# Performance work log

Hardware: AMD Instinct MI355X
Metric: run time of the kernel (lower is better)

The kernel has to match this reference:

```python
import jax, jax.numpy as jnp
import numpy as np

B, N, E = 32, 256, 300   # batch, num hyperedges, word emb size
H, K = 256, 8            # nhidden, nhead
MARGIN = 0.2


def setup_inputs() -> dict:
    key = jax.random.key(0)
    ks = jax.random.split(key, 10)
    s_in = 1.0 / np.sqrt(E)
    s_h = 1.0 / np.sqrt(H)
    s_fc = 1.0 / np.sqrt(H * K)
    return {
        'he_anchor': jax.random.normal(ks[0], (B, N, E), jnp.float32),
        'he_pos': jax.random.normal(ks[1], (B, N, E), jnp.float32),
        'he_neg': jax.random.normal(ks[2], (B, N, E), jnp.float32),
        'W_a2h': jax.random.uniform(ks[3], (H, E), jnp.float32, -s_in, s_in),
        'b_a2h': jax.random.uniform(ks[4], (H,), jnp.float32, -s_in, s_in),
        'W_c2h': jax.random.uniform(ks[5], (H, E), jnp.float32, -s_in, s_in),
        'b_c2h': jax.random.uniform(ks[6], (H,), jnp.float32, -s_in, s_in),
        'W_att': jax.random.uniform(ks[7], (K, H), jnp.float32, -s_h, s_h),
        'b_att': jax.random.uniform(ks[8], (K,), jnp.float32, -s_h, s_h),
        'W_fc': jax.random.uniform(ks[9], (1, H * K), jnp.float32, -s_fc, s_fc),
        'b_fc': jnp.zeros((1,), jnp.float32),
    }


def _score(x, y, W_a2h, b_a2h, W_c2h, b_c2h, W_att, b_att, W_fc, b_fc):
    # a2h / c2h projections, then permute to [B, H, N]
    Aa = jnp.transpose(x @ W_a2h.T + b_a2h, (0, 2, 1))  # [B,H,N]
    Ac = jnp.transpose(y @ W_c2h.T + b_c2h, (0, 2, 1))  # [B,H,M]
    # h2att applied to the outer product Aa[b,h,n]*Ac[b,h,m]; fuse into one einsum
    logits = jnp.einsum('bhn,bhm,kh->bknm', Aa, Ac, W_att) + b_att[None, :, None, None]
    b_, k_, n_, m_ = logits.shape
    att = jax.nn.softmax(logits.reshape(b_, k_, n_ * m_), axis=-1).reshape(b_, k_, n_, m_)
    # per-head bilinear aggregation: out[b,k,h] = sum_{n,m} Aa[b,h,n]*att[b,k,n,m]*Ac[b,h,m]
    t = jnp.einsum('bhn,bknm->bkhm', Aa, att)
    out = jnp.einsum('bkhm,bhm->bkh', t, Ac)
    # torch concat order is head-major: [B, K*H]
    out = out.reshape(b_, k_ * H)
    return out @ W_fc.T + b_fc  # [B,1]


def reference(he_anchor, he_pos, he_neg, W_a2h, b_a2h, W_c2h, b_c2h, W_att, b_att, W_fc, b_fc):
    score_p = _score(he_anchor, he_pos, W_a2h, b_a2h, W_c2h, b_c2h, W_att, b_att, W_fc, b_fc)
    score_n = _score(he_anchor, he_neg, W_a2h, b_a2h, W_c2h, b_c2h, W_att, b_att, W_fc, b_fc)
    loss = jnp.mean(jax.nn.relu(score_n - score_p + MARGIN))
    return loss
```

## Files before the change

kernel.cpp:

```cpp
#include <hip/hip_runtime.h>

#define BB 32
#define NN 256
#define EE 300
#define HH 256
#define KK 8
#define MARGINF 0.2f

typedef __attribute__((ext_vector_type(8))) short bf16x8;
typedef __attribute__((ext_vector_type(4))) float f32x4;
typedef __attribute__((ext_vector_type(16))) float f32x16;

__device__ inline ushort f2bf(float f) {
  unsigned u = __float_as_uint(f);
  u += 0x7fffu + ((u >> 16) & 1u);
  return (ushort)(u >> 16);
}
__device__ inline float bf2f(ushort s) { return __uint_as_float(((unsigned)s) << 16); }
__device__ inline unsigned pack2bf(float f0, float f1) {
  unsigned u0 = __float_as_uint(f0); u0 += 0x7fffu + ((u0 >> 16) & 1u);
  unsigned u1 = __float_as_uint(f1); u1 += 0x7fffu + ((u1 >> 16) & 1u);
  return (u0 >> 16) | (u1 & 0xffff0000u);
}

__global__ __launch_bounds__(256, 3) void proj_kernel(
    const float* __restrict__ he_a, const float* __restrict__ he_p,
    const float* __restrict__ he_n,
    const float* __restrict__ W_a2h, const float* __restrict__ b_a2h,
    const float* __restrict__ W_c2h, const float* __restrict__ b_c2h,
    ushort* __restrict__ AT)
{
  const int z = blockIdx.y;
  const int which = z >> 5;
  const int b = z & 31;
  const int n0 = blockIdx.x * 32;
  const int tid = threadIdx.x;
  const int wv = tid >> 6;
  const int lane = tid & 63;
  const int col = lane & 15;
  const int quad = lane >> 4;

  const float* X = (which == 0 ? he_a : which == 1 ? he_p : he_n) + (size_t)b * NN * EE;
  const float* W = (which == 0 ? W_a2h : W_c2h);
  const float* bias = (which == 0 ? b_a2h : b_c2h);

  __shared__ __align__(16) ushort sX[32][72];
  __shared__ __align__(16) ushort sW[256][72];
  ushort (*tr)[264] = (ushort (*)[264])&sW[0][0];

  f32x4 acc[2][4];
#pragma unroll
  for (int nf = 0; nf < 2; nf++)
#pragma unroll
    for (int mb = 0; mb < 4; mb++) acc[nf][mb] = (f32x4){0.f, 0.f, 0.f, 0.f};

  const int c4 = tid & 15;
  const int rbase = tid >> 4;

  for (int c = 0; c < 5; c++) {
    __syncthreads();
    const int e = 64 * c + 4 * c4;
    const bool ok = (e < 300);
    {
#pragma unroll
      for (int q = 0; q < 2; q++) {
        const int row = rbase + 16 * q;
        float4 xv = {0.f, 0.f, 0.f, 0.f};
        if (ok) xv = *(const float4*)&X[(size_t)(n0 + row) * EE + e];
        uint2 p; p.x = pack2bf(xv.x, xv.y); p.y = pack2bf(xv.z, xv.w);
        *(uint2*)&sX[row][c4 * 4] = p;
      }
    }
    {
#pragma unroll
      for (int q = 0; q < 16; q++) {
        const int row = rbase + 16 * q;
        float4 wf = {0.f, 0.f, 0.f, 0.f};
        if (ok) wf = *(const float4*)&W[(size_t)row * EE + e];
        uint2 p; p.x = pack2bf(wf.x, wf.y); p.y = pack2bf(wf.z, wf.w);
        *(uint2*)&sW[row][c4 * 4] = p;
      }
    }
    __syncthreads();
#pragma unroll
    for (int ks = 0; ks < 2; ks++) {
      const int off = 32 * ks + 8 * quad;
      const bf16x8 a0 = *(const bf16x8*)&sX[col][off];
      const bf16x8 a1 = *(const bf16x8*)&sX[16 + col][off];
#pragma unroll
      for (int mb = 0; mb < 4; mb++) {
        const bf16x8 wb = *(const bf16x8*)&sW[64 * wv + 16 * mb + col][off];
        acc[0][mb] = __builtin_amdgcn_mfma_f32_16x16x32_bf16(a0, wb, acc[0][mb], 0, 0, 0);
        acc[1][mb] = __builtin_amdgcn_mfma_f32_16x16x32_bf16(a1, wb, acc[1][mb], 0, 0, 0);
      }
    }
  }

  __syncthreads();
#pragma unroll
  for (int nf = 0; nf < 2; nf++)
#pragma unroll
    for (int mb = 0; mb < 4; mb++) {
      const float bi = bias[64 * wv + 16 * mb + col];
#pragma unroll
      for (int r = 0; r < 4; r++)
        tr[16 * nf + 4 * quad + r][64 * wv + 16 * mb + col] = f2bf(acc[nf][mb][r] + bi);
    }
  __syncthreads();
  {
    const int row = tid >> 3, seg = tid & 7;
    ushort* dst = &AT[((size_t)(which * BB + b) * NN + n0 + row) * HH];
#pragma unroll
    for (int j = 0; j < 4; j++)
      *(uint4*)&dst[(seg * 4 + j) * 8] = *(const uint4*)&tr[row][(seg * 4 + j) * 8];
  }
}

__global__ __launch_bounds__(256, 2) void attn_kernel(
    const ushort* __restrict__ AT, const float* __restrict__ Watt,
    const float* __restrict__ Wfc, float* __restrict__ scoresK)
{
  const int idx = blockIdx.x;
  const int k = idx >> 6;
  const int g = idx & 63;
  const int which = g >> 5;
  const int b = g & 31;
  const int tid = threadIdx.x;
  const int wv = tid >> 6;
  const int lane = tid & 63;
  const int row32 = lane & 31;
  const int half32 = lane >> 5;

  const ushort* At_a = AT + (size_t)b * NN * HH;
  const ushort* At_c = AT + ((size_t)(1 + which) * BB + b) * NN * HH;
  const uint4* Ac_u4 = (const uint4*)At_c;

  __shared__ __align__(16) ushort sAc[64][264];
  __shared__ __align__(16) float wkf[256];
  __shared__ __align__(16) float wff[256];
  __shared__ float red[8];

  wkf[tid] = Watt[(size_t)k * HH + tid];
  wff[tid] = Wfc[(size_t)k * HH + tid];
  __syncthreads();

  float num = 0.f, den = 0.f;
  const int srow = tid >> 5, scol8 = (tid & 31) * 8;

  for (int s = 0; s < 2; s++) {
    const int nbase = 128 * s + 32 * wv;
    bf16x8 saf[16], gaf[16];
    const ushort* arow = At_a + (size_t)(nbase + row32) * HH;
#pragma unroll
    for (int ks = 0; ks < 16; ks++) {
      const int off = 16 * ks + 8 * half32;
      const bf16x8 a = *(const bf16x8*)&arow[off];
      const float4 wa = *(const float4*)&wkf[off];
      const float4 wb = *(const float4*)&wkf[off + 4];
      const float4 fa = *(const float4*)&wff[off];
      const float4 fb = *(const float4*)&wff[off + 4];
      const float w[8] = {wa.x, wa.y, wa.z, wa.w, wb.x, wb.y, wb.z, wb.w};
      const float f[8] = {fa.x, fa.y, fa.z, fa.w, fb.x, fb.y, fb.z, fb.w};
      union { bf16x8 v; unsigned u[4]; } sv, gv;
#pragma unroll
      for (int jj = 0; jj < 4; jj++) {
        const float a0 = bf2f((ushort)a[2 * jj]), a1 = bf2f((ushort)a[2 * jj + 1]);
        sv.u[jj] = pack2bf(a0 * w[2 * jj], a1 * w[2 * jj + 1]);
        gv.u[jj] = pack2bf(a0 * f[2 * jj], a1 * f[2 * jj + 1]);
      }
      saf[ks] = sv.v; gaf[ks] = gv.v;
    }

    for (int mc = 0; mc < 4; mc++) {
      __syncthreads();
#pragma unroll
      for (int q = 0; q < 8; q++) {
        const int row = q * 8 + srow;
        *(uint4*)&sAc[row][scol8] = Ac_u4[(size_t)(64 * mc + row) * 32 + (tid & 31)];
      }
      __syncthreads();

      f32x16 aS0 = {0,0,0,0,0,0,0,0,0,0,0,0,0,0,0,0};
      f32x16 aS1 = {0,0,0,0,0,0,0,0,0,0,0,0,0,0,0,0};
      f32x16 aG0 = {0,0,0,0,0,0,0,0,0,0,0,0,0,0,0,0};
      f32x16 aG1 = {0,0,0,0,0,0,0,0,0,0,0,0,0,0,0,0};
#pragma unroll
      for (int ks = 0; ks < 16; ks++) {
        const int off = 16 * ks + 8 * half32;
        const bf16x8 b0 = *(const bf16x8*)&sAc[row32][off];
        const bf16x8 b1 = *(const bf16x8*)&sAc[32 + row32][off];
        aS0 = __builtin_amdgcn_mfma_f32_32x32x16_bf16(saf[ks], b0, aS0, 0, 0, 0);
        aG0 = __builtin_amdgcn_mfma_f32_32x32x16_bf16(gaf[ks], b0, aG0, 0, 0, 0);
        aS1 = __builtin_amdgcn_mfma_f32_32x32x16_bf16(saf[ks], b1, aS1, 0, 0, 0);
        aG1 = __builtin_amdgcn_mfma_f32_32x32x16_bf16(gaf[ks], b1, aG1, 0, 0, 0);
      }
#pragma unroll
      for (int r = 0; r < 16; r++) {
        const float p0 = __expf(aS0[r]);
        den += p0; num += p0 * aG0[r];
        const float p1 = __expf(aS1[r]);
        den += p1; num += p1 * aG1[r];
      }
    }
  }

#pragma unroll
  for (int off = 32; off >= 1; off >>= 1) {
    num += __shfl_xor(num, off);
    den += __shfl_xor(den, off);
  }
  if (lane == 0) { red[wv] = num; red[4 + wv] = den; }
  __syncthreads();
  if (tid == 0) {
    const float nt = red[0] + red[1] + red[2] + red[3];
    const float dt = red[4] + red[5] + red[6] + red[7];
    scoresK[idx] = nt / dt;
  }
}

__global__ __launch_bounds__(64) void loss_kernel(
    const float* __restrict__ scoresK, const float* __restrict__ bfc,
    float* __restrict__ out)
{
  const int tid = threadIdx.x;
  float s = bfc[0];
#pragma unroll
  for (int k = 0; k < KK; k++) s += scoresK[k * 64 + tid];
  const float other = __shfl(s, tid + 32);
  float v = 0.f;
  if (tid < 32) v = fmaxf(other - s + MARGINF, 0.f);
#pragma unroll
  for (int off = 32; off >= 1; off >>= 1) v += __shfl_xor(v, off);
  if (tid == 0) out[0] = v * (1.0f / 32.0f);
}

extern "C" void kernel_launch(void* const* d_in, const int* in_sizes, int n_in,
                              void* d_out, int out_size, void* d_ws, size_t ws_size,
                              hipStream_t stream) {
  const float* he_a  = (const float*)d_in[0];
  const float* he_p  = (const float*)d_in[1];
  const float* he_n  = (const float*)d_in[2];
  const float* W_a2h = (const float*)d_in[3];
  const float* b_a2h = (const float*)d_in[4];
  const float* W_c2h = (const float*)d_in[5];
  const float* b_c2h = (const float*)d_in[6];
  const float* W_att = (const float*)d_in[7];
  const float* W_fc  = (const float*)d_in[9];
  const float* b_fc  = (const float*)d_in[10];

  ushort* AT = (ushort*)d_ws;
  float* scoresK = (float*)(AT + (size_t)3 * BB * NN * HH);
  (void)ws_size; (void)in_sizes; (void)n_in; (void)out_size;

  dim3 pg(8, 96);
  proj_kernel<<<pg, 256, 0, stream>>>(he_a, he_p, he_n, W_a2h, b_a2h, W_c2h, b_c2h, AT);
  attn_kernel<<<512, 256, 0, stream>>>(AT, W_att, W_fc, scoresK);
  loss_kernel<<<1, 64, 0, stream>>>(scoresK, b_fc, (float*)d_out);
}
```

Before: 162.8 us.

## Pre-convert projection weights to padded bf16 and read them directly from global

Adds a small kernel that converts W_a2h and W_c2h once per call into a bf16 buffer padded to 320 columns. The projection kernel now loads the whole 32x300 X tile into shared memory up front, then streams weight fragments straight from global/L2 into the MFMAs, with no per-chunk weight staging or barriers. This removes the fp32 weight loads and their conversion, which every one of the 768 blocks used to repeat. The costs are an extra kernel launch, and weight fragments now come from global/L2 with no shared-memory reuse.

```diff
diff --git a/kernel.cpp b/kernel.cpp
--- a/kernel.cpp
+++ b/kernel.cpp
@@ -6,6 +6,7 @@
 #define HH 256
 #define KK 8
 #define MARGINF 0.2f
+#define EP 320
 
 typedef __attribute__((ext_vector_type(8))) short bf16x8;
 typedef __attribute__((ext_vector_type(4))) float f32x4;
@@ -23,11 +24,23 @@
   return (u0 >> 16) | (u1 & 0xffff0000u);
 }
 
+__global__ __launch_bounds__(256) void wconv_kernel(
+    const float* __restrict__ Wa, const float* __restrict__ Wc,
+    ushort* __restrict__ Wb)
+{
+  const int i = blockIdx.x * 256 + threadIdx.x;
+  const int e = i % EP;
+  const int hw = i / EP;
+  const int h = hw & 255;
+  const int w = hw >> 8;
+  const float* src = w ? Wc : Wa;
+  Wb[i] = (e < EE) ? f2bf(src[(size_t)h * EE + e]) : (ushort)0;
+}
+
 __global__ __launch_bounds__(256, 3) void proj_kernel(
     const float* __restrict__ he_a, const float* __restrict__ he_p,
-    const float* __restrict__ he_n,
-    const float* __restrict__ W_a2h, const float* __restrict__ b_a2h,
-    const float* __restrict__ W_c2h, const float* __restrict__ b_c2h,
+    const float* __restrict__ he_n, const ushort* __restrict__ Wb,
+    const float* __restrict__ b_a2h, const float* __restrict__ b_c2h,
     ushort* __restrict__ AT)
 {
   const int z = blockIdx.y;
@@ -41,12 +54,25 @@
   const int quad = lane >> 4;
 
   const float* X = (which == 0 ? he_a : which == 1 ? he_p : he_n) + (size_t)b * NN * EE;
-  const float* W = (which == 0 ? W_a2h : W_c2h);
+  const ushort* W = Wb + (size_t)(which == 0 ? 0 : 1) * HH * EP;
   const float* bias = (which == 0 ? b_a2h : b_c2h);
 
-  __shared__ __align__(16) ushort sX[32][72];
-  __shared__ __align__(16) ushort sW[256][72];
-  ushort (*tr)[264] = (ushort (*)[264])&sW[0][0];
+  __shared__ __align__(16) ushort sX[32][328];
+  __shared__ __align__(16) ushort tr[32][264];
+
+  {
+    const int row = tid >> 3, seg = tid & 7;
+    const float* xr = X + (size_t)(n0 + row) * EE;
+#pragma unroll
+    for (int q = 0; q < 10; q++) {
+      const int j = seg + 8 * q;
+      float4 xv = {0.f, 0.f, 0.f, 0.f};
+      if (j < 75) xv = *(const float4*)&xr[4 * j];
+      uint2 p; p.x = pack2bf(xv.x, xv.y); p.y = pack2bf(xv.z, xv.w);
+      *(uint2*)&sX[row][4 * j] = p;
+    }
+  }
+  __syncthreads();
 
   f32x4 acc[2][4];
 #pragma unroll
@@ -54,49 +80,19 @@
 #pragma unroll
     for (int mb = 0; mb < 4; mb++) acc[nf][mb] = (f32x4){0.f, 0.f, 0.f, 0.f};
 
-  const int c4 = tid & 15;
-  const int rbase = tid >> 4;
-
-  for (int c = 0; c < 5; c++) {
-    __syncthreads();
-    const int e = 64 * c + 4 * c4;
-    const bool ok = (e < 300);
-    {
-#pragma unroll
-      for (int q = 0; q < 2; q++) {
-        const int row = rbase + 16 * q;
-        float4 xv = {0.f, 0.f, 0.f, 0.f};
-        if (ok) xv = *(const float4*)&X[(size_t)(n0 + row) * EE + e];
-        uint2 p; p.x = pack2bf(xv.x, xv.y); p.y = pack2bf(xv.z, xv.w);
-        *(uint2*)&sX[row][c4 * 4] = p;
-      }
-    }
-    {
-#pragma unroll
-      for (int q = 0; q < 16; q++) {
-        const int row = rbase + 16 * q;
-        float4 wf = {0.f, 0.f, 0.f, 0.f};
-        if (ok) wf = *(const float4*)&W[(size_t)row * EE + e];
-        uint2 p; p.x = pack2bf(wf.x, wf.y); p.y = pack2bf(wf.z, wf.w);
-        *(uint2*)&sW[row][c4 * 4] = p;
-      }
-    }
-    __syncthreads();
-#pragma unroll
-    for (int ks = 0; ks < 2; ks++) {
-      const int off = 32 * ks + 8 * quad;
-      const bf16x8 a0 = *(const bf16x8*)&sX[col][off];
-      const bf16x8 a1 = *(const bf16x8*)&sX[16 + col][off];
-#pragma unroll
-      for (int mb = 0; mb < 4; mb++) {
-        const bf16x8 wb = *(const bf16x8*)&sW[64 * wv + 16 * mb + col][off];
-        acc[0][mb] = __builtin_amdgcn_mfma_f32_16x16x32_bf16(a0, wb, acc[0][mb], 0, 0, 0);
-        acc[1][mb] = __builtin_amdgcn_mfma_f32_16x16x32_bf16(a1, wb, acc[1][mb], 0, 0, 0);
-      }
-    }
-  }
-
-  __syncthreads();
+#pragma unroll
+  for (int ks = 0; ks < 10; ks++) {
+    const int off = 32 * ks + 8 * quad;
+    const bf16x8 a0 = *(const bf16x8*)&sX[col][off];
+    const bf16x8 a1 = *(const bf16x8*)&sX[16 + col][off];
+#pragma unroll
+    for (int mb = 0; mb < 4; mb++) {
+      const bf16x8 w8 = *(const bf16x8*)&W[(size_t)(64 * wv + 16 * mb + col) * EP + off];
+      acc[0][mb] = __builtin_amdgcn_mfma_f32_16x16x32_bf16(a0, w8, acc[0][mb], 0, 0, 0);
+      acc[1][mb] = __builtin_amdgcn_mfma_f32_16x16x32_bf16(a1, w8, acc[1][mb], 0, 0, 0);
+    }
+  }
+
 #pragma unroll
   for (int nf = 0; nf < 2; nf++)
 #pragma unroll
@@ -250,10 +246,12 @@
 
   ushort* AT = (ushort*)d_ws;
   float* scoresK = (float*)(AT + (size_t)3 * BB * NN * HH);
+  ushort* Wb = (ushort*)(scoresK + 512);
   (void)ws_size; (void)in_sizes; (void)n_in; (void)out_size;
 
+  wconv_kernel<<<640, 256, 0, stream>>>(W_a2h, W_c2h, Wb);
   dim3 pg(8, 96);
-  proj_kernel<<<pg, 256, 0, stream>>>(he_a, he_p, he_n, W_a2h, b_a2h, W_c2h, b_c2h, AT);
+  proj_kernel<<<pg, 256, 0, stream>>>(he_a, he_p, he_n, Wb, b_a2h, b_c2h, AT);
   attn_kernel<<<512, 256, 0, stream>>>(AT, W_att, W_fc, scoresK);
   loss_kernel<<<1, 64, 0, stream>>>(scoresK, b_fc, (float*)d_out);
 }
```

New measurement: 148.0 us. 9.1% less time.
